# Kernel tuning notes

Measured on AMD Instinct MI355X. Metric: run time of the kernel, lower is better.

The kernel has to match this reference:

```python
import jax, jax.numpy as jnp
import numpy as np

N, V, E = 65536, 2048, 1024
TEMPERATURE = 0.5
EPS = 1e-10
LOG_PARAM_Q = -2.995732273553991


def _l2_normalize(x, axis):
    # matches torch F.normalize(p=2): x / max(||x||, 1e-12)
    n = jnp.sqrt(jnp.sum(x * x, axis=axis, keepdims=True))
    return x / jnp.maximum(n, 1e-12)


def setup_inputs() -> dict:
    key = jax.random.key(0)
    k1, k2, k3 = jax.random.split(key, 3)
    z = jax.random.normal(k1, (N, E), dtype=jnp.float32)
    emb_weight = jax.random.normal(k2, (V, E), dtype=jnp.float32)
    U = jax.random.uniform(k3, (N, V), dtype=jnp.float32)
    return {"z": z, "emb_weight": emb_weight, "U": U}


def reference(z, emb_weight, U):
    kappa_q = jnp.exp(jnp.float32(LOG_PARAM_Q)) + jnp.float32(1.0)
    zn = _l2_normalize(z, axis=1)              # [N, E]
    emb = _l2_normalize(emb_weight, axis=1)    # [V, E]
    # logit = -distances = kappa_q * z @ emb.T
    logit = kappa_q * jnp.matmul(zn, emb.T)    # [N, V]
    # gumbel-softmax sample (training branch)
    g = -jnp.log(-jnp.log(U + EPS) + EPS)
    tokens = jax.nn.softmax((logit + g) / TEMPERATURE, axis=-1)  # [N, V]
    z_q = jnp.matmul(tokens, emb)              # [N, E]
    return (tokens, z_q)
```

## Files before the change

### kernel.cpp

```cpp
#include <hip/hip_runtime.h>
#include <hip/hip_bf16.h>
#include <stdint.h>

typedef short bf16x8 __attribute__((ext_vector_type(8)));
typedef float floatx4 __attribute__((ext_vector_type(4)));

#define N_ROWS 65536
#define V_DIM 2048
#define E_DIM 1024

__device__ __forceinline__ short f2bf(float x) {
  union { float f; uint32_t u; } c; c.f = x;
  uint32_t r = (c.u + 0x7FFFu + ((c.u >> 16) & 1u)) >> 16;
  return (short)(uint16_t)r;
}
__device__ __forceinline__ float bf16f(short b) {
  union { uint32_t u; float f; } c; c.u = ((uint32_t)(uint16_t)b) << 16;
  return c.f;
}
__device__ __forceinline__ uint32_t f2e4m3(float x) {
  union { float f; uint32_t u; } c; c.f = x;
  const uint32_t s = (c.u >> 24) & 0x80u;
  float ax = fabsf(x);
  uint32_t code;
  if (ax < 0.015625f) {
    code = (uint32_t)__float2int_rn(ax * 512.0f);
  } else {
    c.f = ax;
    uint32_t r = c.u + 0x7FFFFu + ((c.u >> 20) & 1u);
    code = (r >> 20) - (120u << 3);
    if (code > 0x7Eu) code = 0x7Eu;
  }
  return s | code;
}

__device__ __forceinline__ float wave_sum(float v) {
#pragma unroll
  for (int o = 32; o > 0; o >>= 1) v += __shfl_xor(v, o);
  return v;
}
__device__ __forceinline__ float wave_max(float v) {
#pragma unroll
  for (int o = 32; o > 0; o >>= 1) v = fmaxf(v, __shfl_xor(v, o));
  return v;
}

__device__ __forceinline__ void gll16(const void* g, void* l) {
  __builtin_amdgcn_global_load_lds(
      (const __attribute__((address_space(1))) void*)g,
      (__attribute__((address_space(3))) void*)l, 16, 0, 0);
}

template <int FAST>
__global__ __launch_bounds__(256) void k_norm_all(
    const float* __restrict__ Z, const float* __restrict__ W,
    short* __restrict__ zn, unsigned char* __restrict__ zn8,
    short* __restrict__ embn, short* __restrict__ embnT,
    unsigned char* __restrict__ embn8) {
  const int t = threadIdx.x;
  const int w = t >> 6, l = t & 63;
  if (blockIdx.x < V_DIM) {
    const int v = blockIdx.x;
    const float4 val = *(const float4*)&W[(size_t)v * E_DIM + t * 4];
    float ss = val.x * val.x + val.y * val.y + val.z * val.z + val.w * val.w;
    ss = wave_sum(ss);
    __shared__ float red[4];
    if (l == 0) red[w] = ss;
    __syncthreads();
    ss = red[0] + red[1] + red[2] + red[3];
    const float inv = 1.0f / fmaxf(sqrtf(ss), 1e-12f);
    short4 o;
    o.x = f2bf(val.x * inv);
    o.y = f2bf(val.y * inv);
    o.z = f2bf(val.z * inv);
    o.w = f2bf(val.w * inv);
    if (!FAST) *(short4*)&embn[(size_t)v * E_DIM + t * 4] = o;
    embnT[(size_t)(t * 4 + 0) * V_DIM + v] = o.x;
    embnT[(size_t)(t * 4 + 1) * V_DIM + v] = o.y;
    embnT[(size_t)(t * 4 + 2) * V_DIM + v] = o.z;
    embnT[(size_t)(t * 4 + 3) * V_DIM + v] = o.w;
    const uint32_t p = f2e4m3(val.x * inv) | (f2e4m3(val.y * inv) << 8) |
                       (f2e4m3(val.z * inv) << 16) | (f2e4m3(val.w * inv) << 24);
    *(uint32_t*)&embn8[(size_t)v * E_DIM + t * 4] = p;
  } else {
    const int row = (blockIdx.x - V_DIM) * 4 + w;
    const float* zr = Z + (size_t)row * E_DIM;
    float4 v[4];
    float ss = 0.f;
#pragma unroll
    for (int i = 0; i < 4; ++i) {
      v[i] = *(const float4*)&zr[(i * 64 + l) * 4];
      ss += v[i].x * v[i].x + v[i].y * v[i].y + v[i].z * v[i].z + v[i].w * v[i].w;
    }
    ss = wave_sum(ss);
    const float SCALE = 2.0f * (expf(-2.995732273553991f) + 1.0f);
    const float inv = SCALE / fmaxf(sqrtf(ss), 1e-12f);
    unsigned char* zo8 = zn8 + (size_t)row * E_DIM;
#pragma unroll
    for (int i = 0; i < 4; ++i) {
      if (!FAST) {
        short4 o;
        o.x = f2bf(v[i].x * inv);
        o.y = f2bf(v[i].y * inv);
        o.z = f2bf(v[i].z * inv);
        o.w = f2bf(v[i].w * inv);
        *(short4*)&zn[(size_t)row * E_DIM + (i * 64 + l) * 4] = o;
      }
      const uint32_t p = f2e4m3(v[i].x * inv) | (f2e4m3(v[i].y * inv) << 8) |
                         (f2e4m3(v[i].z * inv) << 16) | (f2e4m3(v[i].w * inv) << 24);
      *(uint32_t*)&zo8[(i * 64 + l) * 4] = p;
    }
  }
}

__global__ __launch_bounds__(512, 2) void k_gemm_f8(
    const unsigned char* __restrict__ A8, const unsigned char* __restrict__ B8,
    const float* __restrict__ U, short* __restrict__ Pb,
    float* __restrict__ partials, int cpx) {
  __shared__ __align__(16) char Sm[65536];
  const int NT = E_DIM / 32;
  const int tid = threadIdx.x;
  const int wv = tid >> 6, lane = tid & 63;
  const int lr = lane & 15, lh = lane >> 4;
  const int wr = wv >> 2, wc = wv & 3;
  const int d = blockIdx.x;
  const int L = (d & 7) * cpx + (d >> 3);
  const int by = L >> 3, bx = L & 7;
  const int m0 = by * 256, n0 = bx * 256;
  const int sg8 = (((lane & 1) ^ ((lane >> 3) & 1)) << 4);
  const int R8 = tid >> 1;
  const unsigned char* gA = A8 + (size_t)(m0 + R8) * E_DIM + sg8;
  const unsigned char* gB = B8 + (size_t)(n0 + R8) * E_DIM + sg8;
  const int g_ = (lh ^ (((lr >> 2) & 1) << 1)) * 8;
  const int aoff = wr * 4096 + lr * 32 + g_;
  const int boff = wc * 2048 + lr * 32 + g_;

#pragma unroll
  for (int t = 0; t < 2; ++t) {
    gll16(gA + t * 32, Sm + t * 8192 + wv * 1024);
    gll16(gB + t * 32, Sm + 32768 + t * 8192 + wv * 1024);
  }
  asm volatile("s_waitcnt vmcnt(2)" ::: "memory");
  __builtin_amdgcn_s_barrier();
  __builtin_amdgcn_sched_barrier(0);

  floatx4 acc[8][4] = {};

#define DO_TILE(KT, STAGE, VMN)                                                     \
  {                                                                                 \
    const int cb_ = (KT) & 3;                                                       \
    const char* Ab_ = Sm + cb_ * 8192;                                              \
    const char* Bb_ = Sm + 32768 + cb_ * 8192;                                      \
    char* An_ = Sm + (((KT) + 2) & 3) * 8192;                                       \
    char* Bn_ = Sm + 32768 + (((KT) + 2) & 3) * 8192;                               \
    const size_t kc_ = (size_t)((KT) + 2) * 32;                                     \
    long bfr[4], af[4];                                                             \
                  \
    _Pragma("unroll")                                                               \
    for (int n = 0; n < 4; ++n) bfr[n] = *(const long*)(Bb_ + boff + n * 512);      \
    _Pragma("unroll")                                                               \
    for (int i = 0; i < 4; ++i) af[i] = *(const long*)(Ab_ + aoff + i * 512);       \
    if (STAGE) gll16(gA + kc_, An_ + wv * 1024);                                    \
    __builtin_amdgcn_s_barrier();                                                   \
    asm volatile("s_waitcnt lgkmcnt(0)" ::: "memory");                              \
    __builtin_amdgcn_sched_barrier(0);                                              \
    __builtin_amdgcn_s_setprio(1);                                                  \
    _Pragma("unroll")                                                               \
    for (int i = 0; i < 4; ++i) {                                                   \
      _Pragma("unroll")                                                             \
      for (int n = 0; n < 4; ++n)                                                   \
        acc[i][n] =                                                                 \
            __builtin_amdgcn_mfma_f32_16x16x32_fp8_fp8(af[i], bfr[n], acc[i][n], 0, 0, 0); \
    }                                                                               \
    __builtin_amdgcn_s_setprio(0);                                                  \
    __builtin_amdgcn_s_barrier();                                                   \
                             \
    _Pragma("unroll")                                                               \
    for (int i = 0; i < 4; ++i) af[i] = *(const long*)(Ab_ + aoff + 2048 + i * 512);\
    if (STAGE) gll16(gB + kc_, Bn_ + wv * 1024);                                    \
    __builtin_amdgcn_s_barrier();                                                   \
    asm volatile("s_waitcnt lgkmcnt(0)" ::: "memory");                              \
    __builtin_amdgcn_sched_barrier(0);                                              \
    __builtin_amdgcn_s_setprio(1);                                                  \
    _Pragma("unroll")                                                               \
    for (int i = 0; i < 4; ++i) {                                                   \
      _Pragma("unroll")                                                             \
      for (int n = 0; n < 4; ++n)                                                   \
        acc[4 + i][n] =                                                             \
            __builtin_amdgcn_mfma_f32_16x16x32_fp8_fp8(af[i], bfr[n], acc[4 + i][n], 0, 0, 0); \
    }                                                                               \
    __builtin_amdgcn_s_setprio(0);                                                  \
    asm volatile("s_waitcnt vmcnt(" #VMN ")" ::: "memory");                         \
    __builtin_amdgcn_s_barrier();                                                   \
    __builtin_amdgcn_sched_barrier(0);                                              \
  }

  for (int kt = 0; kt < NT - 2; ++kt) DO_TILE(kt, 1, 2);
  DO_TILE(NT - 2, 0, 0);
  DO_TILE(NT - 1, 0, 0);
#undef DO_TILE

  const int gr0 = m0 + wr * 128 + lh * 4;
  const int gc0 = n0 + wc * 64 + lr;
  float rs[8][4] = {};
#pragma unroll
  for (int m = 0; m < 8; ++m)
#pragma unroll
    for (int n = 0; n < 4; ++n) {
      const int col = gc0 + n * 16;
#pragma unroll
      for (int j = 0; j < 4; ++j) {
        const int row = gr0 + m * 16 + j;
        const size_t idx = (size_t)row * V_DIM + col;
        const float u = U[idx];
        const float e = __expf(acc[m][n][j] - 2.f * __logf(-__logf(u + 1e-10f) + 1e-10f));
        const short eb = f2bf(e);
        Pb[idx] = eb;
        rs[m][j] += bf16f(eb);
      }
    }
#pragma unroll
  for (int m = 0; m < 8; ++m)
#pragma unroll
    for (int j = 0; j < 4; ++j) {
      float s = rs[m][j];
      s += __shfl_xor(s, 1); s += __shfl_xor(s, 2);
      s += __shfl_xor(s, 4); s += __shfl_xor(s, 8);
      if (lr == 0)
        partials[(size_t)(gr0 + m * 16 + j) * 32 + bx * 4 + wc] = s;
    }
}

template <int KDIM, int NBX>
__global__ __launch_bounds__(512, 2) void k_gemm8(
    const short* __restrict__ A, const short* __restrict__ B,
    const float* __restrict__ invsum, float* __restrict__ C,
    float* __restrict__ tokens, int cpx) {
  __shared__ __align__(16) short Sm[65536];
  const int NT = KDIM / 32;
  const int tid = threadIdx.x;
  const int wv = tid >> 6, lane = tid & 63;
  const int lr = lane & 15, lh = lane >> 4;
  const int wr = wv >> 2, wc = wv & 3;
  const int d = blockIdx.x;
  const int L = (d & 7) * cpx + (d >> 3);
  const int by = L / NBX, bx = L % NBX;
  const int m0 = by * 256, n0 = bx * 256;
  const int sg = (((lane & 3) ^ ((lane >> 2) & 3) ^ ((lane >> 4) & 3)) << 3);
  const int srow = wv * 16 + (lane >> 2);
  const short* gA = A + (size_t)(m0 + srow) * KDIM + sg;
  const short* gB = B + (size_t)(n0 + srow) * KDIM + sg;
  const int fslot = lh ^ ((lr ^ (lr >> 2)) & 3);
  const int aoff = wr * 8192 + lr * 64 + fslot * 16;
  const int boff = wc * 4096 + lr * 64 + fslot * 16;

  float inv0 = invsum[m0 + srow];
  float inv1 = invsum[m0 + 128 + srow];

#pragma unroll
  for (int t = 0; t < 2; ++t) {
#pragma unroll
    for (int q = 0; q < 2; ++q) {
      gll16(gA + (size_t)(q * 128) * KDIM + t * 32, Sm + t * 8192 + q * 4096 + wv * 512);
      gll16(gB + (size_t)(q * 128) * KDIM + t * 32, Sm + 32768 + t * 8192 + q * 4096 + wv * 512);
    }
  }
  asm volatile("s_waitcnt vmcnt(4)" ::: "memory");
  __builtin_amdgcn_s_barrier();
  __builtin_amdgcn_sched_barrier(0);

  floatx4 acc[8][4] = {};

#define DO_TILE(KT, STAGE, VMN, TOKW_)                                              \
  {                                                                                 \
    const int cb_ = (KT) & 3;                                                       \
    const char* Ab_ = (const char*)Sm + cb_ * 16384;                                \
    const char* Bb_ = (const char*)Sm + 65536 + cb_ * 16384;                        \
    short* An_ = Sm + (((KT) + 2) & 3) * 8192;                                      \
    short* Bn_ = Sm + 32768 + (((KT) + 2) & 3) * 8192;                              \
    const size_t kc_ = (size_t)((KT) + 2) * 32;                                     \
    bf16x8 bfr[4], af[4];                                                           \
    _Pragma("unroll")                                                               \
    for (int n = 0; n < 4; ++n) bfr[n] = *(const bf16x8*)(Bb_ + boff + n * 1024);   \
    _Pragma("unroll")                                                               \
    for (int i = 0; i < 4; ++i) af[i] = *(const bf16x8*)(Ab_ + aoff + i * 1024);    \
    if (STAGE) {                                                                    \
      gll16(gA + kc_, An_ + wv * 512);                                              \
      gll16(gA + (size_t)128 * KDIM + kc_, An_ + 4096 + wv * 512);                  \
    }                                                                               \
    __builtin_amdgcn_s_barrier();                                                   \
    asm volatile("s_waitcnt lgkmcnt(0)" ::: "memory");                              \
    __builtin_amdgcn_sched_barrier(0);                                              \
    __builtin_amdgcn_s_setprio(1);                                                  \
    _Pragma("unroll")                                                               \
    for (int i = 0; i < 4; ++i) {                                                   \
      _Pragma("unroll")                                                             \
      for (int n = 0; n < 4; ++n)                                                   \
        acc[i][n] =                                                                 \
            __builtin_amdgcn_mfma_f32_16x16x32_bf16(af[i], bfr[n], acc[i][n], 0, 0, 0); \
    }                                                                               \
    __builtin_amdgcn_s_setprio(0);                                                  \
    __builtin_amdgcn_s_barrier();                                                   \
    _Pragma("unroll")                                                               \
    for (int i = 0; i < 4; ++i)                                                     \
      af[i] = *(const bf16x8*)(Ab_ + aoff + 4096 + i * 1024);                       \
    if (STAGE) {                                                                    \
      gll16(gB + kc_, Bn_ + wv * 512);                                              \
      gll16(gB + (size_t)128 * KDIM + kc_, Bn_ + 4096 + wv * 512);                  \
    }                                                                               \
    __builtin_amdgcn_s_barrier();                                                   \
    asm volatile("s_waitcnt lgkmcnt(0)" ::: "memory");                              \
    __builtin_amdgcn_sched_barrier(0);                                              \
    __builtin_amdgcn_s_setprio(1);                                                  \
    _Pragma("unroll")                                                               \
    for (int i = 0; i < 4; ++i) {                                                   \
      _Pragma("unroll")                                                             \
      for (int n = 0; n < 4; ++n)                                                   \
        acc[4 + i][n] =                                                             \
            __builtin_amdgcn_mfma_f32_16x16x32_bf16(af[i], bfr[n], acc[4 + i][n], 0, 0, 0); \
    }                                                                               \
    __builtin_amdgcn_s_setprio(0);                                                  \
    if (TOKW_) {                                                                    \
      const short* myA_ = Sm + cb_ * 8192 + wv * 512 + lane * 8;                    \
      const bf16x8 v0_ = *(const bf16x8*)myA_;                                      \
      const bf16x8 v1_ = *(const bf16x8*)(myA_ + 4096);                             \
      const size_t c0_ = (size_t)(KT) * 32 + sg;                                    \
      float4 a_, b_;                                                                \
      a_.x = bf16f(v0_[0]) * inv0; a_.y = bf16f(v0_[1]) * inv0;                     \
      a_.z = bf16f(v0_[2]) * inv0; a_.w = bf16f(v0_[3]) * inv0;                     \
      b_.x = bf16f(v0_[4]) * inv0; b_.y = bf16f(v0_[5]) * inv0;                     \
      b_.z = bf16f(v0_[6]) * inv0; b_.w = bf16f(v0_[7]) * inv0;                     \
      *(float4*)&tokens[(size_t)(m0 + srow) * KDIM + c0_] = a_;                     \
      *(float4*)&tokens[(size_t)(m0 + srow) * KDIM + c0_ + 4] = b_;                 \
      a_.x = bf16f(v1_[0]) * inv1; a_.y = bf16f(v1_[1]) * inv1;                     \
      a_.z = bf16f(v1_[2]) * inv1; a_.w = bf16f(v1_[3]) * inv1;                     \
      b_.x = bf16f(v1_[4]) * inv1; b_.y = bf16f(v1_[5]) * inv1;                     \
      b_.z = bf16f(v1_[6]) * inv1; b_.w = bf16f(v1_[7]) * inv1;                     \
      *(float4*)&tokens[(size_t)(m0 + 128 + srow) * KDIM + c0_] = a_;               \
      *(float4*)&tokens[(size_t)(m0 + 128 + srow) * KDIM + c0_ + 4] = b_;           \
    }                                                                               \
    asm volatile("s_waitcnt vmcnt(" #VMN ")" ::: "memory");                         \
    __builtin_amdgcn_s_barrier();                                                   \
    __builtin_amdgcn_sched_barrier(0);                                              \
  }

  {
    const int s = bx * 16;
    int kt = 0;
    for (; kt < s; ++kt) DO_TILE(kt, 1, 4, 0);
    DO_TILE(kt, 1, 8, 1);
    ++kt;
    for (; kt < s + 16 && kt < NT - 2; ++kt) DO_TILE(kt, 1, 12, 1);
    if (kt == s + 16) {
      DO_TILE(kt, 1, 8, 0);
      ++kt;
    }
    for (; kt < NT - 2; ++kt) DO_TILE(kt, 1, 4, 0);
    DO_TILE(NT - 2, 0, 0, ((NT - 2) >> 4) == bx);
    DO_TILE(NT - 1, 0, 0, ((NT - 1) >> 4) == bx);
  }
#undef DO_TILE

  const int gr0 = m0 + wr * 128 + lh * 4;
  const int gc0 = n0 + wc * 64 + lr;
#pragma unroll
  for (int m = 0; m < 8; ++m)
#pragma unroll
    for (int j = 0; j < 4; ++j) {
      const int row = gr0 + m * 16 + j;
      const float s = invsum[row];
#pragma unroll
      for (int n = 0; n < 4; ++n)
        C[(size_t)row * E_DIM + gc0 + n * 16] = acc[m][n][j] * s;
    }
}

__global__ __launch_bounds__(256) void k_rowsum_inv(const float* __restrict__ partials,
                                                    float* __restrict__ invsum) {
  const int r = blockIdx.x * 256 + threadIdx.x;
  const float4* p = (const float4*)&partials[(size_t)r * 32];
  float s = 0.f;
#pragma unroll
  for (int i = 0; i < 8; ++i) { float4 v = p[i]; s += v.x + v.y + v.z + v.w; }
  invsum[r] = 1.f / s;
}

__global__ __launch_bounds__(256) void k_gemm_nt(const short* __restrict__ A,
                                                 const short* __restrict__ B,
                                                 float* __restrict__ C,
                                                 int lda, int ldb, int ldc, int K) {
  __shared__ __align__(16) short As[128][64];
  __shared__ __align__(16) short Bs[128][64];
  const int t = threadIdx.x;
  const int w = t >> 6, l = t & 63;
  const int lr = l & 15, lh = l >> 4;
  const int m0 = blockIdx.y * 128, n0 = blockIdx.x * 128;
  const int wm = (w >> 1) * 64, wn = (w & 1) * 64;
  floatx4 acc[4][4] = {};
  for (int k0 = 0; k0 < K; k0 += 64) {
    __syncthreads();
#pragma unroll
    for (int i = 0; i < 4; ++i) {
      const int c = i * 256 + t;
      const int r = c >> 3, c8 = (c & 7) * 8;
      *(bf16x8*)&As[r][c8] = *(const bf16x8*)&A[(size_t)(m0 + r) * lda + k0 + c8];
      *(bf16x8*)&Bs[r][c8] = *(const bf16x8*)&B[(size_t)(n0 + r) * ldb + k0 + c8];
    }
    __syncthreads();
#pragma unroll
    for (int kk = 0; kk < 64; kk += 32) {
      bf16x8 af[4], bfr[4];
#pragma unroll
      for (int m = 0; m < 4; ++m) af[m] = *(const bf16x8*)&As[wm + m * 16 + lr][kk + lh * 8];
#pragma unroll
      for (int n = 0; n < 4; ++n) bfr[n] = *(const bf16x8*)&Bs[wn + n * 16 + lr][kk + lh * 8];
#pragma unroll
      for (int m = 0; m < 4; ++m)
#pragma unroll
        for (int n = 0; n < 4; ++n)
          acc[m][n] = __builtin_amdgcn_mfma_f32_16x16x32_bf16(af[m], bfr[n], acc[m][n], 0, 0, 0);
    }
  }
#pragma unroll
  for (int m = 0; m < 4; ++m)
#pragma unroll
    for (int n = 0; n < 4; ++n) {
      const int col = n0 + wn + n * 16 + lr;
#pragma unroll
      for (int j = 0; j < 4; ++j)
        C[(size_t)(m0 + wm + m * 16 + lh * 4 + j) * ldc + col] = acc[m][n][j];
    }
}

__global__ __launch_bounds__(256) void k_gemm_nt_f32a(const float* __restrict__ A,
                                                      const short* __restrict__ B,
                                                      float* __restrict__ C,
                                                      int lda, int ldb, int ldc, int K) {
  __shared__ __align__(16) short As[128][64];
  __shared__ __align__(16) short Bs[128][64];
  const int t = threadIdx.x;
  const int w = t >> 6, l = t & 63;
  const int lr = l & 15, lh = l >> 4;
  const int m0 = blockIdx.y * 128, n0 = blockIdx.x * 128;
  const int wm = (w >> 1) * 64, wn = (w & 1) * 64;
  floatx4 acc[4][4] = {};
  for (int k0 = 0; k0 < K; k0 += 64) {
    __syncthreads();
#pragma unroll
    for (int i = 0; i < 4; ++i) {
      const int c = i * 256 + t;
      const int r = c >> 3, c8 = (c & 7) * 8;
      const float4 a0 = *(const float4*)&A[(size_t)(m0 + r) * lda + k0 + c8];
      const float4 a1 = *(const float4*)&A[(size_t)(m0 + r) * lda + k0 + c8 + 4];
      bf16x8 va;
      va[0] = f2bf(a0.x); va[1] = f2bf(a0.y); va[2] = f2bf(a0.z); va[3] = f2bf(a0.w);
      va[4] = f2bf(a1.x); va[5] = f2bf(a1.y); va[6] = f2bf(a1.z); va[7] = f2bf(a1.w);
      *(bf16x8*)&As[r][c8] = va;
      *(bf16x8*)&Bs[r][c8] = *(const bf16x8*)&B[(size_t)(n0 + r) * ldb + k0 + c8];
    }
    __syncthreads();
#pragma unroll
    for (int kk = 0; kk < 64; kk += 32) {
      bf16x8 af[4], bfr[4];
#pragma unroll
      for (int m = 0; m < 4; ++m) af[m] = *(const bf16x8*)&As[wm + m * 16 + lr][kk + lh * 8];
#pragma unroll
      for (int n = 0; n < 4; ++n) bfr[n] = *(const bf16x8*)&Bs[wn + n * 16 + lr][kk + lh * 8];
#pragma unroll
      for (int m = 0; m < 4; ++m)
#pragma unroll
        for (int n = 0; n < 4; ++n)
          acc[m][n] = __builtin_amdgcn_mfma_f32_16x16x32_bf16(af[m], bfr[n], acc[m][n], 0, 0, 0);
    }
  }
#pragma unroll
  for (int m = 0; m < 4; ++m)
#pragma unroll
    for (int n = 0; n < 4; ++n) {
      const int col = n0 + wn + n * 16 + lr;
#pragma unroll
      for (int j = 0; j < 4; ++j)
        C[(size_t)(m0 + wm + m * 16 + lh * 4 + j) * ldc + col] = acc[m][n][j];
    }
}

__global__ __launch_bounds__(256) void k_gumbel_softmax(float* __restrict__ S,
                                                        const float* __restrict__ U) {
  const int t = threadIdx.x;
  const int w = t >> 6, l = t & 63;
  const size_t base = (size_t)blockIdx.x * V_DIM + t * 8;
  const float4 s0 = *(const float4*)&S[base];
  const float4 s1 = *(const float4*)&S[base + 4];
  const float4 u0 = *(const float4*)&U[base];
  const float4 u1 = *(const float4*)&U[base + 4];
  float x[8];
  x[0] = s0.x - 2.f * __logf(-__logf(u0.x + 1e-10f) + 1e-10f);
  x[1] = s0.y - 2.f * __logf(-__logf(u0.y + 1e-10f) + 1e-10f);
  x[2] = s0.z - 2.f * __logf(-__logf(u0.z + 1e-10f) + 1e-10f);
  x[3] = s0.w - 2.f * __logf(-__logf(u0.w + 1e-10f) + 1e-10f);
  x[4] = s1.x - 2.f * __logf(-__logf(u1.x + 1e-10f) + 1e-10f);
  x[5] = s1.y - 2.f * __logf(-__logf(u1.y + 1e-10f) + 1e-10f);
  x[6] = s1.z - 2.f * __logf(-__logf(u1.z + 1e-10f) + 1e-10f);
  x[7] = s1.w - 2.f * __logf(-__logf(u1.w + 1e-10f) + 1e-10f);
  float lm = x[0];
#pragma unroll
  for (int i = 1; i < 8; ++i) lm = fmaxf(lm, x[i]);
  lm = wave_max(lm);
  __shared__ float redA[4], redB[4];
  if (l == 0) redA[w] = lm;
  __syncthreads();
  const float m = fmaxf(fmaxf(redA[0], redA[1]), fmaxf(redA[2], redA[3]));
  float p[8];
  float ls = 0.f;
#pragma unroll
  for (int i = 0; i < 8; ++i) { p[i] = __expf(x[i] - m); ls += p[i]; }
  ls = wave_sum(ls);
  if (l == 0) redB[w] = ls;
  __syncthreads();
  const float inv = 1.0f / (redB[0] + redB[1] + redB[2] + redB[3]);
  float4 o0 = make_float4(p[0] * inv, p[1] * inv, p[2] * inv, p[3] * inv);
  float4 o1 = make_float4(p[4] * inv, p[5] * inv, p[6] * inv, p[7] * inv);
  *(float4*)&S[base] = o0;
  *(float4*)&S[base + 4] = o1;
}

extern "C" void kernel_launch(void* const* d_in, const int* in_sizes, int n_in,
                              void* d_out, int out_size, void* d_ws, size_t ws_size,
                              hipStream_t stream) {
  const float* z = (const float*)d_in[0];
  const float* W = (const float*)d_in[1];
  const float* U = (const float*)d_in[2];
  float* tokens = (float*)d_out;
  float* zq = tokens + (size_t)N_ROWS * V_DIM;
  short* zn = (short*)zq;
  unsigned char* zn8 =
      (unsigned char*)zq + (size_t)N_ROWS * E_DIM * 2;

  short* embn = (short*)d_ws;
  short* embnT = embn + (size_t)V_DIM * E_DIM;
  unsigned char* embn8 = (unsigned char*)(embnT + (size_t)V_DIM * E_DIM);

  const size_t NEED = (size_t)V_DIM * E_DIM * 2 * 2
                    + (size_t)V_DIM * E_DIM
                    + (size_t)N_ROWS * 32 * 4
                    + (size_t)N_ROWS * 4
                    + (size_t)N_ROWS * V_DIM * 2;

  if (ws_size >= NEED) {
    float* partials = (float*)(embn8 + (size_t)V_DIM * E_DIM);
    float* invsum = partials + (size_t)N_ROWS * 32;
    short* Pb = (short*)(invsum + N_ROWS);
    k_norm_all<1><<<V_DIM + N_ROWS / 4, 256, 0, stream>>>(
        z, W, zn, zn8, embn, embnT, embn8);
    k_gemm_f8<<<2048, 512, 0, stream>>>(zn8, embn8, U, Pb, partials, 2048 / 8);
    k_rowsum_inv<<<N_ROWS / 256, 256, 0, stream>>>(partials, invsum);
    k_gemm8<V_DIM, 4><<<1024, 512, 0, stream>>>(
        Pb, embnT, invsum, zq, tokens, 1024 / 8);
  } else {
    k_norm_all<0><<<V_DIM + N_ROWS / 4, 256, 0, stream>>>(
        z, W, zn, zn8, embn, embnT, embn8);
    k_gemm_nt<<<dim3(V_DIM / 128, N_ROWS / 128), 256, 0, stream>>>(
        zn, embn, tokens, E_DIM, E_DIM, V_DIM, E_DIM);
    k_gumbel_softmax<<<N_ROWS, 256, 0, stream>>>(tokens, U);
    k_gemm_nt_f32a<<<dim3(E_DIM / 128, N_ROWS / 128), 256, 0, stream>>>(
        tokens, embnT, zq, V_DIM, V_DIM, E_DIM, V_DIM);
  }
}
```

Before: 879.5 us.

## Retile fp8 logit GEMM to 256x128 blocks with K=64 triple buffering

Changes the fp8 logit GEMM from 256x256 tiles with K-step 32 and a 4-slot ring to 256x128 tiles with K-step 64 and a 3-stage LDS ring. It uses a 4x2 wave layout with a new XOR swizzle, doubles the grid, and remaps the row-sum partial slots. It also raises the launch bound to 4 blocks per CU to gain more waves for hiding latency. The risks are less data reuse per tile, and register pressure from the tighter launch bound, which could cause spills; 72KB of LDS per block may also stop 4 blocks from fitting on a CU anyway.

After: 846.1 us, median of 2. -3.8%, faster.

```diff
diff --git a/kernel.cpp b/kernel.cpp
--- a/kernel.cpp
+++ b/kernel.cpp
@@ -113,54 +113,59 @@
   }
 }
 
-__global__ __launch_bounds__(512, 2) void k_gemm_f8(
+__global__ __launch_bounds__(512, 4) void k_gemm_f8(
     const unsigned char* __restrict__ A8, const unsigned char* __restrict__ B8,
     const float* __restrict__ U, short* __restrict__ Pb,
     float* __restrict__ partials, int cpx) {
-  __shared__ __align__(16) char Sm[65536];
-  const int NT = E_DIM / 32;
+  __shared__ __align__(16) char Sm[73728];
   const int tid = threadIdx.x;
   const int wv = tid >> 6, lane = tid & 63;
   const int lr = lane & 15, lh = lane >> 4;
-  const int wr = wv >> 2, wc = wv & 3;
+  const int wr = wv >> 1, wc = wv & 1;
   const int d = blockIdx.x;
   const int L = (d & 7) * cpx + (d >> 3);
-  const int by = L >> 3, bx = L & 7;
-  const int m0 = by * 256, n0 = bx * 256;
-  const int sg8 = (((lane & 1) ^ ((lane >> 3) & 1)) << 4);
-  const int R8 = tid >> 1;
-  const unsigned char* gA = A8 + (size_t)(m0 + R8) * E_DIM + sg8;
-  const unsigned char* gB = B8 + (size_t)(n0 + R8) * E_DIM + sg8;
-  const int g_ = (lh ^ (((lr >> 2) & 1) << 1)) * 8;
-  const int aoff = wr * 4096 + lr * 32 + g_;
-  const int boff = wc * 2048 + lr * 32 + g_;
+  const int by = L >> 4, bx = L & 15;
+  const int m0 = by * 256, n0 = bx * 128;
+  const int sg8 = (((tid & 3) ^ ((tid >> 2) & 3)) << 4);
+  const unsigned char* gA = A8 + (size_t)(m0 + (tid >> 2)) * E_DIM + sg8;
+  const unsigned char* gB = B8 + (size_t)(n0 + (tid >> 2)) * E_DIM + sg8;
+  const int t3 = lr & 3;
+  const int soff0 = ((((lh >> 1) + 0) ^ t3) << 4) + (lh & 1) * 8;
+  const int soff1 = ((((lh >> 1) + 2) ^ t3) << 4) + (lh & 1) * 8;
+  const int arow = (wr * 64 + lr) * 64;
+  const int brow = (wc * 64 + lr) * 64;
 
 #pragma unroll
   for (int t = 0; t < 2; ++t) {
-    gll16(gA + t * 32, Sm + t * 8192 + wv * 1024);
-    gll16(gB + t * 32, Sm + 32768 + t * 8192 + wv * 1024);
-  }
-  asm volatile("s_waitcnt vmcnt(2)" ::: "memory");
+    char* sa = Sm + t * 16384;
+    char* sb = Sm + 49152 + t * 8192;
+    gll16(gA + t * 64, sa + wv * 1024);
+    gll16(gA + (size_t)128 * E_DIM + t * 64, sa + 8192 + wv * 1024);
+    gll16(gB + t * 64, sb + wv * 1024);
+  }
+  asm volatile("s_waitcnt vmcnt(3)" ::: "memory");
   __builtin_amdgcn_s_barrier();
   __builtin_amdgcn_sched_barrier(0);
 
-  floatx4 acc[8][4] = {};
-
-#define DO_TILE(KT, STAGE, VMN)                                                     \
+  floatx4 acc[4][4] = {};
+
+#define DO_TILE(KT, CB, SN, STAGE, VMN)                                             \
   {                                                                                 \
-    const int cb_ = (KT) & 3;                                                       \
-    const char* Ab_ = Sm + cb_ * 8192;                                              \
-    const char* Bb_ = Sm + 32768 + cb_ * 8192;                                      \
-    char* An_ = Sm + (((KT) + 2) & 3) * 8192;                                       \
-    char* Bn_ = Sm + 32768 + (((KT) + 2) & 3) * 8192;                               \
-    const size_t kc_ = (size_t)((KT) + 2) * 32;                                     \
+    const char* Ab_ = Sm + (CB) * 16384;                                            \
+    const char* Bb_ = Sm + 49152 + (CB) * 8192;                                     \
+    char* An_ = Sm + (SN) * 16384;                                                  \
+    char* Bn_ = Sm + 49152 + (SN) * 8192;                                           \
+    const size_t kc_ = (size_t)((KT) + 2) * 64;                                     \
     long bfr[4], af[4];                                                             \
-                  \
-    _Pragma("unroll")                                                               \
-    for (int n = 0; n < 4; ++n) bfr[n] = *(const long*)(Bb_ + boff + n * 512);      \
-    _Pragma("unroll")                                                               \
-    for (int i = 0; i < 4; ++i) af[i] = *(const long*)(Ab_ + aoff + i * 512);       \
-    if (STAGE) gll16(gA + kc_, An_ + wv * 1024);                                    \
+                \
+    _Pragma("unroll")                                                               \
+    for (int n = 0; n < 4; ++n) bfr[n] = *(const long*)(Bb_ + brow + n * 1024 + soff0); \
+    _Pragma("unroll")                                                               \
+    for (int i = 0; i < 4; ++i) af[i] = *(const long*)(Ab_ + arow + i * 1024 + soff0); \
+    if (STAGE) {                                                                    \
+      gll16(gA + kc_, An_ + wv * 1024);                                             \
+      gll16(gA + (size_t)128 * E_DIM + kc_, An_ + 8192 + wv * 1024);                \
+    }                                                                               \
     __builtin_amdgcn_s_barrier();                                                   \
     asm volatile("s_waitcnt lgkmcnt(0)" ::: "memory");                              \
     __builtin_amdgcn_sched_barrier(0);                                              \
@@ -174,9 +179,11 @@
     }                                                                               \
     __builtin_amdgcn_s_setprio(0);                                                  \
     __builtin_amdgcn_s_barrier();                                                   \
-                             \
-    _Pragma("unroll")                                                               \
-    for (int i = 0; i < 4; ++i) af[i] = *(const long*)(Ab_ + aoff + 2048 + i * 512);\
+                           \
+    _Pragma("unroll")                                                               \
+    for (int n = 0; n < 4; ++n) bfr[n] = *(const long*)(Bb_ + brow + n * 1024 + soff1); \
+    _Pragma("unroll")                                                               \
+    for (int i = 0; i < 4; ++i) af[i] = *(const long*)(Ab_ + arow + i * 1024 + soff1); \
     if (STAGE) gll16(gB + kc_, Bn_ + wv * 1024);                                    \
     __builtin_amdgcn_s_barrier();                                                   \
     asm volatile("s_waitcnt lgkmcnt(0)" ::: "memory");                              \
@@ -186,8 +193,8 @@
     for (int i = 0; i < 4; ++i) {                                                   \
       _Pragma("unroll")                                                             \
       for (int n = 0; n < 4; ++n)                                                   \
-        acc[4 + i][n] =                                                             \
-            __builtin_amdgcn_mfma_f32_16x16x32_fp8_fp8(af[i], bfr[n], acc[4 + i][n], 0, 0, 0); \
+        acc[i][n] =                                                                 \
+            __builtin_amdgcn_mfma_f32_16x16x32_fp8_fp8(af[i], bfr[n], acc[i][n], 0, 0, 0); \
     }                                                                               \
     __builtin_amdgcn_s_setprio(0);                                                  \
     asm volatile("s_waitcnt vmcnt(" #VMN ")" ::: "memory");                         \
@@ -195,16 +202,22 @@
     __builtin_amdgcn_sched_barrier(0);                                              \
   }
 
-  for (int kt = 0; kt < NT - 2; ++kt) DO_TILE(kt, 1, 2);
-  DO_TILE(NT - 2, 0, 0);
-  DO_TILE(NT - 1, 0, 0);
+  for (int kt = 0; kt < 12; kt += 3) {
+    DO_TILE(kt + 0, 0, 2, 1, 3);
+    DO_TILE(kt + 1, 1, 0, 1, 3);
+    DO_TILE(kt + 2, 2, 1, 1, 3);
+  }
+  DO_TILE(12, 0, 2, 1, 3);
+  DO_TILE(13, 1, 0, 1, 3);
+  DO_TILE(14, 2, 0, 0, 0);
+  DO_TILE(15, 0, 0, 0, 0);
 #undef DO_TILE
 
-  const int gr0 = m0 + wr * 128 + lh * 4;
+  const int gr0 = m0 + wr * 64 + lh * 4;
   const int gc0 = n0 + wc * 64 + lr;
-  float rs[8][4] = {};
-#pragma unroll
-  for (int m = 0; m < 8; ++m)
+  float rs[4][4] = {};
+#pragma unroll
+  for (int m = 0; m < 4; ++m)
 #pragma unroll
     for (int n = 0; n < 4; ++n) {
       const int col = gc0 + n * 16;
@@ -220,14 +233,14 @@
       }
     }
 #pragma unroll
-  for (int m = 0; m < 8; ++m)
+  for (int m = 0; m < 4; ++m)
 #pragma unroll
     for (int j = 0; j < 4; ++j) {
       float s = rs[m][j];
       s += __shfl_xor(s, 1); s += __shfl_xor(s, 2);
       s += __shfl_xor(s, 4); s += __shfl_xor(s, 8);
       if (lr == 0)
-        partials[(size_t)(gr0 + m * 16 + j) * 32 + bx * 4 + wc] = s;
+        partials[(size_t)(gr0 + m * 16 + j) * 32 + bx * 2 + wc] = s;
     }
 }
 
@@ -552,7 +565,7 @@
     short* Pb = (short*)(invsum + N_ROWS);
     k_norm_all<1><<<V_DIM + N_ROWS / 4, 256, 0, stream>>>(
         z, W, zn, zn8, embn, embnT, embn8);
-    k_gemm_f8<<<2048, 512, 0, stream>>>(zn8, embn8, U, Pb, partials, 2048 / 8);
+    k_gemm_f8<<<4096, 512, 0, stream>>>(zn8, embn8, U, Pb, partials, 4096 / 8);
     k_rowsum_inv<<<N_ROWS / 256, 256, 0, stream>>>(partials, invsum);
     k_gemm8<V_DIM, 4><<<1024, 512, 0, stream>>>(
         Pb, embnT, invsum, zq, tokens, 1024 / 8);
```
